# Kernel tuning notes

Measured on AMD Instinct MI355X. Metric: run time of the kernel, lower is better.

The kernel has to match this reference:

```python
import jax, jax.numpy as jnp
import numpy as np

N_NODES = 50000
N_EDGES = 1600000
N_GRAPHS = 64


def _gcn_conv(x, row, col, ew, W, b, n_nodes):
    # x: [N, Fin] -> [N, Fout]; PyG GCNConv: lin, add self-loops (w=1),
    # symmetric normalization, scatter-add at target (col), + bias.
    x = x @ W
    loop = jnp.arange(n_nodes, dtype=row.dtype)
    r = jnp.concatenate([row, loop])
    c = jnp.concatenate([col, loop])
    w = jnp.concatenate([ew, jnp.ones((n_nodes,), dtype=ew.dtype)])
    deg = jax.ops.segment_sum(w, c, num_segments=n_nodes)
    dinv = jnp.where(deg > 0, jax.lax.rsqrt(jnp.where(deg > 0, deg, 1.0)), 0.0)
    norm = dinv[r] * w * dinv[c]                      # [E+N]
    msg = x[r] * norm[:, None]                        # [E+N, Fout] (dominant traffic)
    out = jax.ops.segment_sum(msg, c, num_segments=n_nodes)
    return out + b


def setup_inputs() -> dict:
    key = jax.random.key(0)
    ks = jax.random.split(key, 12)
    x = jax.random.normal(ks[0], (N_NODES, 128), dtype=jnp.float32)
    edge_index = jax.random.randint(ks[1], (2, N_EDGES), 0, N_NODES, dtype=jnp.int32)
    edge_attr = jax.random.uniform(ks[2], (N_EDGES,), dtype=jnp.float32)
    batch = jnp.sort(jax.random.randint(ks[3], (N_NODES,), 0, N_GRAPHS, dtype=jnp.int32))
    glorot = lambda k, fi, fo: jax.random.normal(k, (fi, fo), jnp.float32) * np.sqrt(2.0 / (fi + fo))
    return {
        "x": x, "edge_index": edge_index, "edge_attr": edge_attr, "batch": batch,
        "W1": glorot(ks[4], 128, 128), "b1": jnp.zeros((128,), jnp.float32),
        "W2": glorot(ks[5], 128, 64), "b2": jnp.zeros((64,), jnp.float32),
        "fc1_W": glorot(ks[6], 64, 128), "fc1_b": jnp.zeros((128,), jnp.float32),
        "fc2_W": glorot(ks[7], 128, 2), "fc2_b": jnp.zeros((2,), jnp.float32),
    }


def reference(x, edge_index, edge_attr, batch, W1, b1, W2, b2, fc1_W, fc1_b, fc2_W, fc2_b):
    row, col = edge_index[0], edge_index[1]
    h = jax.nn.relu(_gcn_conv(x, row, col, edge_attr, W1, b1, N_NODES))
    x1 = jax.nn.relu(_gcn_conv(h, row, col, edge_attr, W2, b2, N_NODES))
    # global mean pool over batch ids
    sums = jax.ops.segment_sum(x1, batch, num_segments=N_GRAPHS)
    cnt = jax.ops.segment_sum(jnp.ones((N_NODES,), x1.dtype), batch, num_segments=N_GRAPHS)
    x2 = sums / jnp.maximum(cnt, 1.0)[:, None]        # [B, 64]
    # dropout is identity in eval mode
    h = jax.nn.relu(x2 @ fc1_W + fc1_b)
    logits = h @ fc2_W + fc2_b                        # [B, 2]
    return jax.nn.log_softmax(logits, axis=1)
```

## Files before the change

kernel.cpp:

```cpp
#include <hip/hip_runtime.h>
#include <hip/hip_bf16.h>


#define CAP 64
#define OVFCAP 8192
#define MAXNR 6400
#define PCH 32
#define BSTR 68
#define KP 136

typedef float v2f  __attribute__((ext_vector_type(2)));
typedef float f32x4 __attribute__((ext_vector_type(4)));
typedef short bf16x8 __attribute__((ext_vector_type(8)));

__device__ inline unsigned short f2bf(float f) {
    unsigned u = __float_as_uint(f);
    u += 0x7FFFu + ((u >> 16) & 1u);
    return (unsigned short)(u >> 16);
}
__device__ inline void fp8x4_to_f32(unsigned w, float* o) {
    v2f lo = __builtin_amdgcn_cvt_pk_f32_fp8((int)w, false);
    v2f hi = __builtin_amdgcn_cvt_pk_f32_fp8((int)w, true);
    o[0] = lo[0]; o[1] = lo[1]; o[2] = hi[0]; o[3] = hi[1];
}
__device__ inline unsigned f32x4_to_fp8(float a, float b, float c, float d) {
    int w = 0;
    w = __builtin_amdgcn_cvt_pk_fp8_f32(a, b, w, false);
    w = __builtin_amdgcn_cvt_pk_fp8_f32(c, d, w, true);
    return (unsigned)w;
}

__global__ void prepw_kernel(const float* __restrict__ W1, const float* __restrict__ W2,
                             unsigned short* __restrict__ wt1, unsigned short* __restrict__ wt2) {
    int t = threadIdx.x;
    if (blockIdx.x == 0) {
        for (int i = t; i < 128 * 128; i += 256) {
            int c = i >> 7, k = i & 127;
            wt1[c * KP + k] = f2bf(W1[k * 128 + c]);
        }
    } else {
        for (int i = t; i < 64 * 128; i += 256) {
            int c = i >> 7, k = i & 127;
            wt2[c * KP + k] = f2bf(W2[k * 64 + c]);
        }
    }
}

__global__ void part_kernel(const int* __restrict__ rows, const int* __restrict__ cols,
                            const float* __restrict__ ew, int* __restrict__ rangeCnt,
                            uint2* __restrict__ rng, int E, int NR, int RSEG) {
    __shared__ int hc[8];
    const int t = threadIdx.x;
    const int nb = gridDim.x;
    const int CS = (E + nb - 1) / nb;
    const int e0 = blockIdx.x * CS, e1 = min(e0 + CS, E);
    if (t < 8) hc[t] = 0;
    __syncthreads();
    for (int e = e0 + t; e < e1; e += 256) {
        int r = cols[e] / NR;
        atomicAdd(&hc[r], 1);
    }
    __syncthreads();
    if (t < 8) hc[t] = atomicAdd(&rangeCnt[t], hc[t]);
    __syncthreads();
    for (int e = e0 + t; e < e1; e += 256) {
        int c = cols[e];
        int r = c / NR;
        int q = (int)(ew[e] * 32768.0f);
        if (q > 32767) q = 32767;
        unsigned rec = ((unsigned)rows[e] << 15) | (unsigned)q;
        int pos = atomicAdd(&hc[r], 1);
        if (pos < RSEG) rng[(size_t)r * RSEG + pos] = make_uint2((unsigned)c, rec);
    }
}

__global__ __launch_bounds__(1024)
void hist2_kernel(const uint2* __restrict__ rng, const int* __restrict__ rangeCnt,
                  int* __restrict__ h2d, int* __restrict__ w2d, int NR, int RSEG) {
    __shared__ int hist[MAXNR];
    __shared__ int wsum[MAXNR];
    const int r = blockIdx.x & 7, j = blockIdx.x >> 3;
    const int t = threadIdx.x;
    const int M = min(rangeCnt[r], RSEG);
    const int CS = (M + PCH - 1) / PCH;
    const int e0 = j * CS, e1 = min(e0 + CS, M);
    for (int n = t; n < NR; n += 1024) { hist[n] = 0; wsum[n] = 0; }
    __syncthreads();
    const uint2* lst = rng + (size_t)r * RSEG;
    for (int k = e0 + t; k < e1; k += 1024) {
        unsigned c = lst[k].x - r * NR;
        atomicAdd(&hist[c], 1);
        atomicAdd(&wsum[c], (int)(lst[k].y & 32767u));
    }
    __syncthreads();
    int* dst = h2d + (size_t)(r * PCH + j) * NR;
    int* wdst = w2d + (size_t)(r * PCH + j) * NR;
    for (int n = t; n < NR; n += 1024) { dst[n] = hist[n]; wdst[n] = wsum[n]; }
}

__global__ void scan2_kernel(int* __restrict__ h2d, const int* __restrict__ w2d,
                             int* __restrict__ cnt, float* __restrict__ dinv, int NR, int N) {
    int n = blockIdx.x * 256 + threadIdx.x;
    if (n >= N) return;
    int r = n / NR, c = n - r * NR;
    int* col = h2d + (size_t)(r * PCH) * NR + c;
    const int* wcol = w2d + (size_t)(r * PCH) * NR + c;
    int run = 0;
    long long ws = 0;
    #pragma unroll 8
    for (int j = 0; j < PCH; ++j) {
        int v = col[(size_t)j * NR];
        col[(size_t)j * NR] = run;
        run += v;
        ws += wcol[(size_t)j * NR];
    }
    cnt[n] = run;
    dinv[n] = rsqrtf((float)ws * (1.0f / 32768.0f) + 1.0f);
}

__global__ __launch_bounds__(1024)
void place2_kernel(const uint2* __restrict__ rng, const int* __restrict__ rangeCnt,
                   const int* __restrict__ h2d, unsigned* __restrict__ slot,
                   int4* __restrict__ ovf, int* __restrict__ ovfcnt,
                   int NR, int RSEG) {
    __shared__ int cur[MAXNR];
    const int r = blockIdx.x & 7, j = blockIdx.x >> 3;
    const int t = threadIdx.x;
    const int M = min(rangeCnt[r], RSEG);
    const int CS = (M + PCH - 1) / PCH;
    const int e0 = j * CS, e1 = min(e0 + CS, M);
    const int* src = h2d + (size_t)(r * PCH + j) * NR;
    for (int n = t; n < NR; n += 1024) cur[n] = src[n];
    __syncthreads();
    const uint2* lst = rng + (size_t)r * RSEG;
    for (int k = e0 + t; k < e1; k += 1024) {
        uint2 u2 = lst[k];
        int pos = atomicAdd(&cur[u2.x - r * NR], 1);
        if (pos < CAP) {
            slot[(size_t)u2.x * CAP + pos] = u2.y;
        } else {
            int o = atomicAdd(ovfcnt, 1);
            if (o < OVFCAP)
                ovf[o] = make_int4((int)(u2.y >> 15), (int)u2.x, (int)(u2.y & 32767u), 0);
        }
    }
}

__global__ void place_simple_kernel(const int* __restrict__ rows, const int* __restrict__ cols,
                                    const float* __restrict__ ew, int* __restrict__ cnt,
                                    unsigned* __restrict__ slot, int4* __restrict__ ovf,
                                    int* __restrict__ ovfcnt, int E) {
    int e = blockIdx.x * 256 + threadIdx.x;
    if (e >= E) return;
    int r = rows[e], c = cols[e];
    int q = (int)(ew[e] * 32768.0f);
    if (q > 32767) q = 32767;
    int pos = atomicAdd(&cnt[c], 1);
    if (pos < CAP) {
        slot[(size_t)c * CAP + pos] = ((unsigned)r << 15) | (unsigned)q;
    } else {
        int o = atomicAdd(ovfcnt, 1);
        if (o < OVFCAP) ovf[o] = make_int4(r, c, q, 0);
    }
}

__global__ void degfin_kernel(const unsigned* __restrict__ slot, const int* __restrict__ cnt,
                              const int4* __restrict__ ovf, const int* __restrict__ ovfcnt,
                              float* __restrict__ dinv, int N) {
    const int w = threadIdx.x >> 6, lane = threadIdx.x & 63;
    const int i = blockIdx.x * 4 + w;
    if (i >= N) return;
    int mraw = cnt[i];
    int m = mraw > CAP ? CAP : mraw;
    float v = 0.f;
    if (lane < m) v = (float)(slot[(size_t)i * CAP + lane] & 32767u);
    if (mraw > CAP) {
        int oc = *ovfcnt; if (oc > OVFCAP) oc = OVFCAP;
        for (int k = lane; k < oc; k += 64)
            if (ovf[k].y == i) v += (float)ovf[k].z;
    }
    #pragma unroll
    for (int off = 1; off < 64; off <<= 1) v += __shfl_xor(v, off);
    if (lane == 0) dinv[i] = rsqrtf(v * (1.0f / 32768.0f) + 1.0f);
}

template <int BN, bool AF32>
__global__ __launch_bounds__(256)
void gemm_mfma_kernel(const void* __restrict__ Av, const unsigned short* __restrict__ wt,
                      const float* __restrict__ dinv, unsigned char* __restrict__ outf8,
                      int M) {
    constexpr int CT = BN / 16;
    constexpr int EPS = BN + 4;
    __shared__ unsigned short wl[BN * KP];
    __shared__ float ep[4][16 * EPS];
    const int t = threadIdx.x;
    for (int i = t; i < BN * KP / 8; i += 256)
        ((uint4*)wl)[i] = ((const uint4*)wt)[i];
    __syncthreads();
    const int w = t >> 6, lane = t & 63;
    const int n16 = lane & 15, q = lane >> 4;
    const int rowBase = blockIdx.x * 64 + w * 16;
    int arow = rowBase + n16; if (arow >= M) arow = M - 1;
    f32x4 acc[CT];
    #pragma unroll
    for (int ct = 0; ct < CT; ++ct) acc[ct] = (f32x4){0.f, 0.f, 0.f, 0.f};
    #pragma unroll
    for (int kt = 0; kt < 4; ++kt) {
        bf16x8 af;
        if (AF32) {
            const float* ap = (const float*)Av + (size_t)arow * 128 + kt * 32 + q * 8;
            float4 a0 = *(const float4*)ap;
            float4 a1 = *(const float4*)(ap + 4);
            af[0] = (short)f2bf(a0.x); af[1] = (short)f2bf(a0.y);
            af[2] = (short)f2bf(a0.z); af[3] = (short)f2bf(a0.w);
            af[4] = (short)f2bf(a1.x); af[5] = (short)f2bf(a1.y);
            af[6] = (short)f2bf(a1.z); af[7] = (short)f2bf(a1.w);
        } else {
            af = *(const bf16x8*)((const unsigned short*)Av + (size_t)arow * 128 + kt * 32 + q * 8);
        }
        #pragma unroll
        for (int ct = 0; ct < CT; ++ct) {
            bf16x8 bfr = *(const bf16x8*)&wl[(ct * 16 + n16) * KP + kt * 32 + q * 8];
            acc[ct] = __builtin_amdgcn_mfma_f32_16x16x32_bf16(af, bfr, acc[ct], 0, 0, 0);
        }
    }
    #pragma unroll
    for (int ct = 0; ct < CT; ++ct)
        #pragma unroll
        for (int r = 0; r < 4; ++r)
            ep[w][(q * 4 + r) * EPS + ct * 16 + n16] = acc[ct][r];
    __syncthreads();
    const int lr = lane & 15;
    const int cc = (lane >> 4) * (BN / 4);
    int grow = rowBase + lr;
    if (grow < M) {
        float s = dinv[grow];
        const float* src = &ep[w][lr * EPS + cc];
        #pragma unroll
        for (int u = 0; u < BN / 64; ++u) {
            int col0 = cc + u * 16;
            int slice = col0 >> 6, cw = col0 & 63;
            unsigned w0 = f32x4_to_fp8(src[u*16+ 0]*s, src[u*16+ 1]*s, src[u*16+ 2]*s, src[u*16+ 3]*s);
            unsigned w1 = f32x4_to_fp8(src[u*16+ 4]*s, src[u*16+ 5]*s, src[u*16+ 6]*s, src[u*16+ 7]*s);
            unsigned w2 = f32x4_to_fp8(src[u*16+ 8]*s, src[u*16+ 9]*s, src[u*16+10]*s, src[u*16+11]*s);
            unsigned w3 = f32x4_to_fp8(src[u*16+12]*s, src[u*16+13]*s, src[u*16+14]*s, src[u*16+15]*s);
            *(uint4*)&outf8[((size_t)slice * M + grow) * 64 + cw] = make_uint4(w0, w1, w2, w3);
        }
    }
}

template <int F, int S, bool OB>
__global__ void gather_kernel(const unsigned char* __restrict__ xsb,
                              const unsigned* __restrict__ slot,
                              const int* __restrict__ cnt, const float* __restrict__ dinv,
                              const float* __restrict__ b, const int4* __restrict__ ovf,
                              const int* __restrict__ ovfcnt, void* __restrict__ outv, int N) {
    constexpr int EPN = 4;
    __shared__ unsigned sbkt[16 * BSTR];
    const int slice = (S > 1) ? ((int)blockIdx.x % S) : 0;
    const int grp = (S > 1) ? ((int)blockIdx.x / S) : blockIdx.x;
    const int t = threadIdx.x;
    const int node0 = grp * 16;
    {
        int ndl = t >> 4, part = t & 15;
        int snode = node0 + ndl; if (snode >= N) snode = N - 1;
        *(uint4*)&sbkt[ndl * BSTR + part * 4] =
            *(const uint4*)&slot[(size_t)snode * CAP + part * 4];
    }
    __syncthreads();
    const int w = t >> 6, lane = t & 63;
    const int cg = lane & 3;
    const int e  = (lane >> 2) & 3;
    const int nd = lane >> 4;
    const int ndl = w * 4 + nd;
    const int i = node0 + ndl;
    const bool iv = (i < N);
    const int ic = iv ? i : 0;
    const uint4* xs4 = (const uint4*)(xsb + (size_t)slice * N * 64);
    int mraw = iv ? cnt[ic] : 0;
    int m = mraw > CAP ? CAP : mraw;
    const unsigned* lb = &sbkt[ndl * BSTR];
    float acc[16] = {};
    int j = e;
    for (; j + EPN < m; j += 2 * EPN) {
        unsigned u0 = lb[j], u1 = lb[j + EPN];
        float c0 = (float)(u0 & 32767u), c1 = (float)(u1 & 32767u);
        uint4 a0 = xs4[(size_t)(u0 >> 15) * 4 + cg];
        uint4 a1 = xs4[(size_t)(u1 >> 15) * 4 + cg];
        float f0[16], f1[16];
        fp8x4_to_f32(a0.x, f0 + 0);  fp8x4_to_f32(a0.y, f0 + 4);
        fp8x4_to_f32(a0.z, f0 + 8);  fp8x4_to_f32(a0.w, f0 + 12);
        fp8x4_to_f32(a1.x, f1 + 0);  fp8x4_to_f32(a1.y, f1 + 4);
        fp8x4_to_f32(a1.z, f1 + 8);  fp8x4_to_f32(a1.w, f1 + 12);
        #pragma unroll
        for (int k = 0; k < 16; ++k) acc[k] += f0[k] * c0 + f1[k] * c1;
    }
    if (j < m) {
        unsigned u = lb[j];
        float c = (float)(u & 32767u);
        uint4 a = xs4[(size_t)(u >> 15) * 4 + cg];
        float f[16];
        fp8x4_to_f32(a.x, f + 0);  fp8x4_to_f32(a.y, f + 4);
        fp8x4_to_f32(a.z, f + 8);  fp8x4_to_f32(a.w, f + 12);
        #pragma unroll
        for (int k = 0; k < 16; ++k) acc[k] += f[k] * c;
    }
    if (mraw > CAP) {
        int oc = *ovfcnt; if (oc > OVFCAP) oc = OVFCAP;
        for (int k = e; k < oc; k += EPN) {
            int4 r4 = ovf[k];
            if (r4.y == i) {
                float c = (float)r4.z;
                uint4 a = xs4[(size_t)r4.x * 4 + cg];
                float f[16];
                fp8x4_to_f32(a.x, f + 0);  fp8x4_to_f32(a.y, f + 4);
                fp8x4_to_f32(a.z, f + 8);  fp8x4_to_f32(a.w, f + 12);
                #pragma unroll
                for (int kk = 0; kk < 16; ++kk) acc[kk] += f[kk] * c;
            }
        }
    }
    #pragma unroll
    for (int k = 0; k < 16; ++k) {
        acc[k] += __shfl_xor(acc[k], 4);
        acc[k] += __shfl_xor(acc[k], 8);
    }
    if (e == 0 && iv) {
        float d = dinv[i];
        float sa = d * (1.0f / 32768.0f);
        uint4 sv = xs4[(size_t)i * 4 + cg];
        float sf[16];
        fp8x4_to_f32(sv.x, sf + 0);  fp8x4_to_f32(sv.y, sf + 4);
        fp8x4_to_f32(sv.z, sf + 8);  fp8x4_to_f32(sv.w, sf + 12);
        const float* bb = &b[slice * 64 + cg * 16];
        float o[16];
        #pragma unroll
        for (int k = 0; k < 16; ++k)
            o[k] = fmaxf(acc[k] * sa + sf[k] * d + bb[k], 0.f);
        if (OB) {
            unsigned short* dst = (unsigned short*)outv + (size_t)i * F + slice * 64 + cg * 16;
            unsigned pw[8];
            #pragma unroll
            for (int k = 0; k < 8; ++k)
                pw[k] = (unsigned)f2bf(o[2 * k]) | ((unsigned)f2bf(o[2 * k + 1]) << 16);
            *(uint4*)&dst[0] = make_uint4(pw[0], pw[1], pw[2], pw[3]);
            *(uint4*)&dst[8] = make_uint4(pw[4], pw[5], pw[6], pw[7]);
        } else {
            float* dst = (float*)outv + (size_t)i * F + slice * 64 + cg * 16;
            *(float4*)&dst[0]  = make_float4(o[0], o[1], o[2], o[3]);
            *(float4*)&dst[4]  = make_float4(o[4], o[5], o[6], o[7]);
            *(float4*)&dst[8]  = make_float4(o[8], o[9], o[10], o[11]);
            *(float4*)&dst[12] = make_float4(o[12], o[13], o[14], o[15]);
        }
    }
}

__global__ void pool_kernel(const float* __restrict__ x1, const int* __restrict__ batch,
                            float* __restrict__ sums, float* __restrict__ cnt, int N) {
    constexpr int QG = 16, S = 16, ITER = 16;
    int t = threadIdx.x;
    int q = t % QG, s = t / QG;
    int n0 = blockIdx.x * (S * ITER) + s * ITER;
    float4 acc = make_float4(0.f, 0.f, 0.f, 0.f);
    float cacc = 0.f;
    int gcur = -1;
    for (int i = 0; i < ITER; ++i) {
        int n = n0 + i;
        if (n >= N) break;
        int gid = batch[n];
        if (gid != gcur) {
            if (gcur >= 0) {
                float* dst = &sums[gcur * 64 + q * 4];
                atomicAdd(dst + 0, acc.x);
                atomicAdd(dst + 1, acc.y);
                atomicAdd(dst + 2, acc.z);
                atomicAdd(dst + 3, acc.w);
                if (q == 0) atomicAdd(&cnt[gcur], cacc);
            }
            gcur = gid;
            acc = make_float4(0.f, 0.f, 0.f, 0.f);
            cacc = 0.f;
        }
        float4 a = ((const float4*)x1)[n * QG + q];
        acc.x += a.x; acc.y += a.y; acc.z += a.z; acc.w += a.w;
        if (q == 0) cacc += 1.f;
    }
    if (gcur >= 0) {
        float* dst = &sums[gcur * 64 + q * 4];
        atomicAdd(dst + 0, acc.x);
        atomicAdd(dst + 1, acc.y);
        atomicAdd(dst + 2, acc.z);
        atomicAdd(dst + 3, acc.w);
        if (q == 0) atomicAdd(&cnt[gcur], cacc);
    }
}

__global__ void head_kernel(const float* __restrict__ sums, const float* __restrict__ cnt,
                            const float* __restrict__ fc1W, const float* __restrict__ fc1b,
                            const float* __restrict__ fc2W, const float* __restrict__ fc2b,
                            float* __restrict__ out) {
    __shared__ float x2s[64];
    __shared__ float hs[128];
    __shared__ float lg[2];
    const int g = blockIdx.x;
    const int t = threadIdx.x;
    if (t < 64) {
        float c = fmaxf(cnt[g], 1.f);
        x2s[t] = sums[g * 64 + t] / c;
    }
    __syncthreads();
    {
        float a = fc1b[t];
        #pragma unroll 8
        for (int j = 0; j < 64; ++j) a += x2s[j] * fc1W[j * 128 + t];
        hs[t] = fmaxf(a, 0.f);
    }
    __syncthreads();
    {
        int m = t >> 6, l = t & 63;
        float p = hs[l] * fc2W[l * 2 + m] + hs[l + 64] * fc2W[(l + 64) * 2 + m];
        #pragma unroll
        for (int off = 1; off < 64; off <<= 1) p += __shfl_xor(p, off);
        if (l == 0) lg[m] = p + fc2b[m];
    }
    __syncthreads();
    if (t == 0) {
        float l0 = lg[0], l1 = lg[1];
        float mx = fmaxf(l0, l1);
        float lse = mx + logf(expf(l0 - mx) + expf(l1 - mx));
        out[g * 2 + 0] = l0 - lse;
        out[g * 2 + 1] = l1 - lse;
    }
}

extern "C" void kernel_launch(void* const* d_in, const int* in_sizes, int n_in,
                              void* d_out, int out_size, void* d_ws, size_t ws_size,
                              hipStream_t stream) {
    const float* x      = (const float*)d_in[0];
    const int*   eidx   = (const int*)d_in[1];
    const float* ew     = (const float*)d_in[2];
    const int*   batch  = (const int*)d_in[3];
    const float* W1     = (const float*)d_in[4];
    const float* b1     = (const float*)d_in[5];
    const float* W2     = (const float*)d_in[6];
    const float* b2     = (const float*)d_in[7];
    const float* fc1W   = (const float*)d_in[8];
    const float* fc1b   = (const float*)d_in[9];
    const float* fc2W   = (const float*)d_in[10];
    const float* fc2b   = (const float*)d_in[11];
    float* out = (float*)d_out;

    const int N = in_sizes[3];
    const int E = in_sizes[2];
    const int G = 64;
    const int* rows = eidx;
    const int* cols = eidx + E;
    const int NR = (N + 7) / 8;
    const int RSEG = E / 8 + 32768;

    float* ws = (float*)d_ws;
    size_t off = 0;
    auto alloc = [&](size_t n) { float* p = ws + off; off += (n + 15) & ~(size_t)15; return p; };
    float*    sums     = alloc(64 * 64);
    float*    cntf     = alloc(16);
    int*      ovfcnt   = (int*)alloc(16);
    int*      rangeCnt = (int*)alloc(16);
    int*      cnt      = (int*)alloc(N);
    size_t zfloats = off;
    float*    dinv   = alloc(N);
    unsigned short* wt1 = (unsigned short*)alloc(128 * KP / 2 + 16);
    unsigned short* wt2 = (unsigned short*)alloc(64 * KP / 2 + 16);
    unsigned* slot   = (unsigned*)alloc((size_t)N * CAP);
    int4*     ovf    = (int4*)alloc((size_t)OVFCAP * 4);
    float*    bufA   = alloc((size_t)N * 128);
    float*    bufB   = alloc((size_t)N * 128);
    int*            h2d   = (int*)bufA;
    int*            w2d   = h2d + (size_t)8 * PCH * NR;
    unsigned char*  xw1f8 = (unsigned char*)bufA;
    unsigned char*  xw2f8 = (unsigned char*)bufA;
    float*          x1    = bufA + (size_t)N * 32;
    uint2*          rng   = (uint2*)bufB;
    unsigned short* hbf   = (unsigned short*)bufB;
    (void)ws_size;

    hipMemsetAsync(d_ws, 0, zfloats * sizeof(float), stream);

    prepw_kernel<<<2, 256, 0, stream>>>(W1, W2, wt1, wt2);

    if (NR <= MAXNR) {
        part_kernel<<<256, 256, 0, stream>>>(rows, cols, ew, rangeCnt, rng, E, NR, RSEG);
        hist2_kernel<<<8 * PCH, 1024, 0, stream>>>(rng, rangeCnt, h2d, w2d, NR, RSEG);
        scan2_kernel<<<(N + 255) / 256, 256, 0, stream>>>(h2d, w2d, cnt, dinv, NR, N);
        place2_kernel<<<8 * PCH, 1024, 0, stream>>>(rng, rangeCnt, h2d, slot, ovf, ovfcnt, NR, RSEG);
    } else {
        place_simple_kernel<<<(E + 255) / 256, 256, 0, stream>>>(rows, cols, ew, cnt, slot, ovf, ovfcnt, E);
        degfin_kernel<<<(N + 3) / 4, 256, 0, stream>>>(slot, cnt, ovf, ovfcnt, dinv, N);
    }

    gemm_mfma_kernel<128, true><<<(N + 63) / 64, 256, 0, stream>>>(x, wt1, dinv, xw1f8, N);
    gather_kernel<128, 2, true><<<((N + 15) / 16) * 2, 256, 0, stream>>>(xw1f8, slot, cnt, dinv, b1, ovf, ovfcnt, hbf, N);

    gemm_mfma_kernel<64, false><<<(N + 63) / 64, 256, 0, stream>>>(hbf, wt2, dinv, xw2f8, N);
    gather_kernel<64, 1, false><<<(N + 15) / 16, 256, 0, stream>>>(xw2f8, slot, cnt, dinv, b2, ovf, ovfcnt, x1, N);

    pool_kernel<<<(N + 255) / 256, 256, 0, stream>>>(x1, batch, sums, cntf, N);
    head_kernel<<<G, 128, 0, stream>>>(sums, cntf, fc1W, fc1b, fc2W, fc2b, out);
}
```

Baseline: 258.9 us.

## Fuse mean-pool into second gather and weight prep into partition kernel

Global mean pooling now happens inside the second gather kernel. Each block stages its 16 node outputs in shared memory and performs segmented atomic adds into the per-graph sums and counts, so x1 is no longer written to global memory and reread by a separate pool kernel. Weight transpose and bf16 conversion move into two extra blocks of the partition kernel, removing one launch. The slot-list load now skips entries beyond each node's edge count. The trade-off is more atomics per block, 16 nodes instead of 256, and the fallback path now runs the partition kernel unnecessarily.

New measurement: 239.6 us. 7.5% less time.

```diff
diff --git a/kernel.cpp b/kernel.cpp
--- a/kernel.cpp
+++ b/kernel.cpp
@@ -8,6 +8,7 @@
 #define PCH 32
 #define BSTR 68
 #define KP 136
+#define PARTNB 256
 
 typedef float v2f  __attribute__((ext_vector_type(2)));
 typedef float f32x4 __attribute__((ext_vector_type(4)));
@@ -30,29 +31,28 @@
     return (unsigned)w;
 }
 
-__global__ void prepw_kernel(const float* __restrict__ W1, const float* __restrict__ W2,
-                             unsigned short* __restrict__ wt1, unsigned short* __restrict__ wt2) {
-    int t = threadIdx.x;
-    if (blockIdx.x == 0) {
-        for (int i = t; i < 128 * 128; i += 256) {
-            int c = i >> 7, k = i & 127;
-            wt1[c * KP + k] = f2bf(W1[k * 128 + c]);
-        }
-    } else {
-        for (int i = t; i < 64 * 128; i += 256) {
-            int c = i >> 7, k = i & 127;
-            wt2[c * KP + k] = f2bf(W2[k * 64 + c]);
-        }
-    }
-}
-
 __global__ void part_kernel(const int* __restrict__ rows, const int* __restrict__ cols,
                             const float* __restrict__ ew, int* __restrict__ rangeCnt,
-                            uint2* __restrict__ rng, int E, int NR, int RSEG) {
+                            uint2* __restrict__ rng, int E, int NR, int RSEG,
+                            const float* __restrict__ W1, const float* __restrict__ W2,
+                            unsigned short* __restrict__ wt1, unsigned short* __restrict__ wt2) {
+    const int t = threadIdx.x;
+    if (blockIdx.x >= PARTNB) {
+        if (blockIdx.x == PARTNB) {
+            for (int i = t; i < 128 * 128; i += 256) {
+                int c = i >> 7, k = i & 127;
+                wt1[c * KP + k] = f2bf(W1[k * 128 + c]);
+            }
+        } else {
+            for (int i = t; i < 64 * 128; i += 256) {
+                int c = i >> 7, k = i & 127;
+                wt2[c * KP + k] = f2bf(W2[k * 64 + c]);
+            }
+        }
+        return;
+    }
     __shared__ int hc[8];
-    const int t = threadIdx.x;
-    const int nb = gridDim.x;
-    const int CS = (E + nb - 1) / nb;
+    const int CS = (E + PARTNB - 1) / PARTNB;
     const int e0 = blockIdx.x * CS, e1 = min(e0 + CS, E);
     if (t < 8) hc[t] = 0;
     __syncthreads();
@@ -249,14 +249,18 @@
     }
 }
 
-template <int F, int S, bool OB>
+template <int F, int S, bool OB, bool POOL>
 __global__ void gather_kernel(const unsigned char* __restrict__ xsb,
                               const unsigned* __restrict__ slot,
                               const int* __restrict__ cnt, const float* __restrict__ dinv,
                               const float* __restrict__ b, const int4* __restrict__ ovf,
-                              const int* __restrict__ ovfcnt, void* __restrict__ outv, int N) {
+                              const int* __restrict__ ovfcnt, void* __restrict__ outv, int N,
+                              const int* __restrict__ gbatch, float* __restrict__ gsums,
+                              float* __restrict__ gcnt) {
     constexpr int EPN = 4;
     __shared__ unsigned sbkt[16 * BSTR];
+    __shared__ float x1s[16 * 68];
+    __shared__ int gidl[16];
     const int slice = (S > 1) ? ((int)blockIdx.x % S) : 0;
     const int grp = (S > 1) ? ((int)blockIdx.x / S) : blockIdx.x;
     const int t = threadIdx.x;
@@ -264,8 +268,16 @@
     {
         int ndl = t >> 4, part = t & 15;
         int snode = node0 + ndl; if (snode >= N) snode = N - 1;
-        *(uint4*)&sbkt[ndl * BSTR + part * 4] =
-            *(const uint4*)&slot[(size_t)snode * CAP + part * 4];
+        int sc = cnt[snode]; if (sc > CAP) sc = CAP;
+        if (part * 4 < sc)
+            *(uint4*)&sbkt[ndl * BSTR + part * 4] =
+                *(const uint4*)&slot[(size_t)snode * CAP + part * 4];
+    }
+    if constexpr (POOL) {
+        if (t < 16) {
+            int sn = node0 + t;
+            gidl[t] = (sn < N) ? gbatch[sn] : -1;
+        }
     }
     __syncthreads();
     const int w = t >> 6, lane = t & 63;
@@ -345,53 +357,49 @@
                 pw[k] = (unsigned)f2bf(o[2 * k]) | ((unsigned)f2bf(o[2 * k + 1]) << 16);
             *(uint4*)&dst[0] = make_uint4(pw[0], pw[1], pw[2], pw[3]);
             *(uint4*)&dst[8] = make_uint4(pw[4], pw[5], pw[6], pw[7]);
-        } else {
+        } else if constexpr (!POOL) {
             float* dst = (float*)outv + (size_t)i * F + slice * 64 + cg * 16;
             *(float4*)&dst[0]  = make_float4(o[0], o[1], o[2], o[3]);
             *(float4*)&dst[4]  = make_float4(o[4], o[5], o[6], o[7]);
             *(float4*)&dst[8]  = make_float4(o[8], o[9], o[10], o[11]);
             *(float4*)&dst[12] = make_float4(o[12], o[13], o[14], o[15]);
-        }
-    }
-}
-
-__global__ void pool_kernel(const float* __restrict__ x1, const int* __restrict__ batch,
-                            float* __restrict__ sums, float* __restrict__ cnt, int N) {
-    constexpr int QG = 16, S = 16, ITER = 16;
-    int t = threadIdx.x;
-    int q = t % QG, s = t / QG;
-    int n0 = blockIdx.x * (S * ITER) + s * ITER;
-    float4 acc = make_float4(0.f, 0.f, 0.f, 0.f);
-    float cacc = 0.f;
-    int gcur = -1;
-    for (int i = 0; i < ITER; ++i) {
-        int n = n0 + i;
-        if (n >= N) break;
-        int gid = batch[n];
-        if (gid != gcur) {
-            if (gcur >= 0) {
-                float* dst = &sums[gcur * 64 + q * 4];
-                atomicAdd(dst + 0, acc.x);
-                atomicAdd(dst + 1, acc.y);
-                atomicAdd(dst + 2, acc.z);
-                atomicAdd(dst + 3, acc.w);
-                if (q == 0) atomicAdd(&cnt[gcur], cacc);
+        } else {
+            float* dst = &x1s[ndl * 68 + cg * 16];
+            *(float4*)&dst[0]  = make_float4(o[0], o[1], o[2], o[3]);
+            *(float4*)&dst[4]  = make_float4(o[4], o[5], o[6], o[7]);
+            *(float4*)&dst[8]  = make_float4(o[8], o[9], o[10], o[11]);
+            *(float4*)&dst[12] = make_float4(o[12], o[13], o[14], o[15]);
+        }
+    }
+    if constexpr (POOL) {
+        __syncthreads();
+        if (t < 64) {
+            const int f = t;
+            float run = 0.f; int gcur = -1;
+            #pragma unroll 4
+            for (int n = 0; n < 16; ++n) {
+                int g = gidl[n];
+                if (g < 0) break;
+                if (g != gcur) {
+                    if (gcur >= 0) atomicAdd(&gsums[gcur * 64 + f], run);
+                    run = 0.f; gcur = g;
+                }
+                run += x1s[n * 68 + f];
             }
-            gcur = gid;
-            acc = make_float4(0.f, 0.f, 0.f, 0.f);
-            cacc = 0.f;
-        }
-        float4 a = ((const float4*)x1)[n * QG + q];
-        acc.x += a.x; acc.y += a.y; acc.z += a.z; acc.w += a.w;
-        if (q == 0) cacc += 1.f;
-    }
-    if (gcur >= 0) {
-        float* dst = &sums[gcur * 64 + q * 4];
-        atomicAdd(dst + 0, acc.x);
-        atomicAdd(dst + 1, acc.y);
-        atomicAdd(dst + 2, acc.z);
-        atomicAdd(dst + 3, acc.w);
-        if (q == 0) atomicAdd(&cnt[gcur], cacc);
+            if (gcur >= 0) atomicAdd(&gsums[gcur * 64 + f], run);
+        } else if (t == 64) {
+            float rc = 0.f; int gcur = -1;
+            for (int n = 0; n < 16; ++n) {
+                int g = gidl[n];
+                if (g < 0) break;
+                if (g != gcur) {
+                    if (gcur >= 0) atomicAdd(&gcnt[gcur], rc);
+                    rc = 0.f; gcur = g;
+                }
+                rc += 1.f;
+            }
+            if (gcur >= 0) atomicAdd(&gcnt[gcur], rc);
+        }
     }
 }
 
@@ -478,31 +486,32 @@
     int*            w2d   = h2d + (size_t)8 * PCH * NR;
     unsigned char*  xw1f8 = (unsigned char*)bufA;
     unsigned char*  xw2f8 = (unsigned char*)bufA;
-    float*          x1    = bufA + (size_t)N * 32;
     uint2*          rng   = (uint2*)bufB;
     unsigned short* hbf   = (unsigned short*)bufB;
     (void)ws_size;
 
     hipMemsetAsync(d_ws, 0, zfloats * sizeof(float), stream);
 
-    prepw_kernel<<<2, 256, 0, stream>>>(W1, W2, wt1, wt2);
-
     if (NR <= MAXNR) {
-        part_kernel<<<256, 256, 0, stream>>>(rows, cols, ew, rangeCnt, rng, E, NR, RSEG);
+        part_kernel<<<PARTNB + 2, 256, 0, stream>>>(rows, cols, ew, rangeCnt, rng, E, NR, RSEG,
+                                                    W1, W2, wt1, wt2);
         hist2_kernel<<<8 * PCH, 1024, 0, stream>>>(rng, rangeCnt, h2d, w2d, NR, RSEG);
         scan2_kernel<<<(N + 255) / 256, 256, 0, stream>>>(h2d, w2d, cnt, dinv, NR, N);
         place2_kernel<<<8 * PCH, 1024, 0, stream>>>(rng, rangeCnt, h2d, slot, ovf, ovfcnt, NR, RSEG);
     } else {
+        part_kernel<<<PARTNB + 2, 256, 0, stream>>>(rows, cols, ew, rangeCnt, rng, E, NR, RSEG,
+                                                    W1, W2, wt1, wt2);
         place_simple_kernel<<<(E + 255) / 256, 256, 0, stream>>>(rows, cols, ew, cnt, slot, ovf, ovfcnt, E);
         degfin_kernel<<<(N + 3) / 4, 256, 0, stream>>>(slot, cnt, ovf, ovfcnt, dinv, N);
     }
 
     gemm_mfma_kernel<128, true><<<(N + 63) / 64, 256, 0, stream>>>(x, wt1, dinv, xw1f8, N);
-    gather_kernel<128, 2, true><<<((N + 15) / 16) * 2, 256, 0, stream>>>(xw1f8, slot, cnt, dinv, b1, ovf, ovfcnt, hbf, N);
+    gather_kernel<128, 2, true, false><<<((N + 15) / 16) * 2, 256, 0, stream>>>(
+        xw1f8, slot, cnt, dinv, b1, ovf, ovfcnt, hbf, N, nullptr, nullptr, nullptr);
 
     gemm_mfma_kernel<64, false><<<(N + 63) / 64, 256, 0, stream>>>(hbf, wt2, dinv, xw2f8, N);
-    gather_kernel<64, 1, false><<<(N + 15) / 16, 256, 0, stream>>>(xw2f8, slot, cnt, dinv, b2, ovf, ovfcnt, x1, N);
-
-    pool_kernel<<<(N + 255) / 256, 256, 0, stream>>>(x1, batch, sums, cntf, N);
+    gather_kernel<64, 1, false, true><<<(N + 15) / 16, 256, 0, stream>>>(
+        xw2f8, slot, cnt, dinv, b2, ovf, ovfcnt, nullptr, N, batch, sums, cntf);
+
     head_kernel<<<G, 128, 0, stream>>>(sums, cntf, fc1W, fc1b, fc2W, fc2b, out);
 }
```
